# Kernel optimization log

Measured on AMD Instinct MI355X. Metric: run time of the kernel, lower is better.

## Reference

```python
import jax, jax.numpy as jnp
import numpy as np

N = 50000; F = 128; H = 128; E = 800000; G = 512; C = 1000; CE = 64; L = 128
EPS = 1e-5

def gcn_conv(x, src, dst, W, b, num_nodes):
    # PyG GCNConv: add self loops, sym-normalize, aggregate at dst
    loop = jnp.arange(num_nodes)
    s = jnp.concatenate([src, loop])
    d = jnp.concatenate([dst, loop])
    deg = jax.ops.segment_sum(jnp.ones_like(d, dtype=x.dtype), d, num_segments=num_nodes)
    dinv = jnp.where(deg > 0, jax.lax.rsqrt(deg), 0.0)
    norm = dinv[s] * dinv[d]                      # [E+N]
    h = x @ W                                     # [N,H]
    msg = h[s] * norm[:, None]                    # gather + scale
    return jax.ops.segment_sum(msg, d, num_segments=num_nodes) + b

def layer_norm(x, w, b):
    mu = jnp.mean(x, axis=-1, keepdims=True)
    var = jnp.var(x, axis=-1, keepdims=True)
    return (x - mu) * jax.lax.rsqrt(var + EPS) * w + b

def setup_inputs() -> dict:
    key = jax.random.key(0)
    ks = jax.random.split(key, 16)
    x = jax.random.normal(ks[0], (N, F), dtype=jnp.float32)
    edge_index = jax.random.randint(ks[1], (2, E), 0, N)
    batch = jnp.sort(jax.random.randint(ks[2], (N,), 0, G))
    cell_lines = jax.random.randint(ks[3], (G,), 0, C)
    def kai(k, shape):
        fan_in = shape[0]
        bound = np.sqrt(6.0 / fan_in)
        return jax.random.uniform(k, shape, jnp.float32, -bound, bound)
    return {
        'x': x, 'edge_index': edge_index, 'batch': batch, 'cell_lines': cell_lines,
        'W1': kai(ks[4], (F, H)), 'b1': jnp.zeros((H,), jnp.float32),
        'W2': kai(ks[5], (H, H)), 'b2': jnp.zeros((H,), jnp.float32),
        'emb': jax.random.normal(ks[6], (C, CE), dtype=jnp.float32),
        'Wc': kai(ks[7], (H + CE, H)), 'bc': jnp.zeros((H,), jnp.float32),
        'lnc_w': jnp.ones((H,), jnp.float32), 'lnc_b': jnp.zeros((H,), jnp.float32),
        'Wf1': kai(ks[8], (H, H)), 'bf1': jnp.zeros((H,), jnp.float32),
        'ln1_w': jnp.ones((H,), jnp.float32), 'ln1_b': jnp.zeros((H,), jnp.float32),
        'Wf2': kai(ks[9], (H, L)), 'bf2': jnp.zeros((L,), jnp.float32),
    }

def reference(x, edge_index, batch, cell_lines, W1, b1, W2, b2, emb, Wc, bc,
              lnc_w, lnc_b, Wf1, bf1, ln1_w, ln1_b, Wf2, bf2):
    src, dst = edge_index[0], edge_index[1]
    h = jax.nn.relu(gcn_conv(x, src, dst, W1, b1, N))
    h = jax.nn.relu(gcn_conv(h, src, dst, W2, b2, N))
    g = jax.ops.segment_sum(h, batch, num_segments=G)          # global_add_pool [G,H]
    ce = emb[cell_lines]                                       # [G,CE]
    comb = jnp.concatenate([g, ce], axis=1)
    comb = jax.nn.relu(layer_norm(comb @ Wc + bc, lnc_w, lnc_b))
    out = jax.nn.relu(comb @ Wf1 + bf1)                        # dropout = identity (eval)
    out = layer_norm(out, ln1_w, ln1_b)
    return out @ Wf2 + bf2
```

## Files before the change

### kernel.cpp

```cpp
#include <hip/hip_runtime.h>

#define N_NODES 50000
#define NFEAT 128
#define NEDGE 800000
#define NGRAPH 512
#define NCE 64
#define EPS 1e-5f
#define NBUCK 196
#define EPB 4096
#define BCAP 6144

typedef short s8v __attribute__((ext_vector_type(8)));
typedef float f4v __attribute__((ext_vector_type(4)));
typedef float f2v __attribute__((ext_vector_type(2)));

static __device__ __forceinline__ unsigned short f2bf(float f) {
    unsigned int u = __float_as_uint(f);
    unsigned int r = u + 0x7fffu + ((u >> 16) & 1u);
    return (unsigned short)(r >> 16);
}
static __device__ __forceinline__ float bf_lo(unsigned int packed) {
    return __uint_as_float(packed << 16);
}
static __device__ __forceinline__ float bf_hi(unsigned int packed) {
    return __uint_as_float(packed & 0xffff0000u);
}
static __device__ __forceinline__ float bf_us(unsigned short us) {
    return __uint_as_float(((unsigned int)us) << 16);
}
static __device__ __forceinline__ f2v unpk(unsigned int u) {
    f2v r; r.x = bf_lo(u); r.y = bf_hi(u); return r;
}

__global__ __launch_bounds__(256) void wcast_kernel(
    const float* __restrict__ W1, const float* __restrict__ W2,
    unsigned short* __restrict__ WT1, unsigned short* __restrict__ WT2,
    int* __restrict__ bucketCursor)
{
    if (blockIdx.x == 0 && blockIdx.y == 0 && threadIdx.x < NBUCK)
        bucketCursor[threadIdx.x] = 0;
    const float* W = blockIdx.y ? W2 : W1;
    unsigned short* WT = blockIdx.y ? WT2 : WT1;
    int idx = blockIdx.x * 256 + threadIdx.x;
    int k = idx >> 7, n = idx & 127;
    WT[n * 128 + k] = f2bf(W[idx]);
}

__global__ __launch_bounds__(256) void bucket_scatter_kernel(
    const int* __restrict__ ei, int* __restrict__ bucketCursor,
    unsigned int* __restrict__ recbuf, int E)
{
    __shared__ int hist[NBUCK];
    __shared__ int lbase[NBUCK];
    __shared__ int gbase[NBUCK];
    __shared__ int cur[NBUCK];
    __shared__ int scanbuf[256];
    __shared__ unsigned int staging[EPB];
    int tid = threadIdx.x;
    if (tid < NBUCK) { hist[tid] = 0; cur[tid] = 0; }
    __syncthreads();

    unsigned int rec[EPB / 256];
    int e0 = blockIdx.x * EPB + tid;
#pragma unroll
    for (int i = 0; i < EPB / 256; ++i) {
        int e = e0 + i * 256;
        if (e < E) {
            unsigned int sv = (unsigned)ei[e];
            unsigned int dv = (unsigned)ei[E + e];
            rec[i] = sv | (dv << 16);
            atomicAdd(&hist[dv >> 8], 1);
        } else {
            rec[i] = 0xffffffffu;
        }
    }
    __syncthreads();
    int v = (tid < NBUCK) ? hist[tid] : 0;
    scanbuf[tid] = v; __syncthreads();
    for (int off = 1; off < 256; off <<= 1) {
        int t = (tid >= off) ? scanbuf[tid - off] : 0;
        __syncthreads();
        scanbuf[tid] += t;
        __syncthreads();
    }
    if (tid < NBUCK) lbase[tid] = scanbuf[tid] - v;
    int total = scanbuf[255];
    if (tid < NBUCK) gbase[tid] = (v > 0) ? atomicAdd(&bucketCursor[tid], v) : 0;
    __syncthreads();
#pragma unroll
    for (int i = 0; i < EPB / 256; ++i) {
        if (rec[i] != 0xffffffffu) {
            int b = rec[i] >> 24;
            int loc = atomicAdd(&cur[b], 1);
            staging[lbase[b] + loc] = rec[i];
        }
    }
    __syncthreads();
    for (int s = tid; s < total; s += 256) {
        unsigned int r = staging[s];
        int b = r >> 24;
        int pos = gbase[b] + (s - lbase[b]);
        if (pos < BCAP) recbuf[(size_t)b * BCAP + pos] = r;
    }
}

__global__ __launch_bounds__(256) void bucket_csr_kernel(
    const unsigned int* __restrict__ recbuf, const int* __restrict__ bucketCursor,
    int* __restrict__ rowbeg, unsigned short* __restrict__ deg,
    float* __restrict__ dinv, unsigned short* __restrict__ colidx)
{
    __shared__ int cnt[256];
    __shared__ int cur[256];
    __shared__ int scanbuf[256];
    __shared__ unsigned short stage[BCAP];
    int b = blockIdx.x, tid = threadIdx.x;
    int base = b * BCAP;
    int len = bucketCursor[b]; if (len > BCAP) len = BCAP;
    cnt[tid] = 0;
    __syncthreads();
    for (int s = tid; s < len; s += 256) {
        unsigned int r = recbuf[base + s];
        atomicAdd(&cnt[(r >> 16) & 255], 1);
    }
    __syncthreads();
    int v = cnt[tid];
    scanbuf[tid] = v; __syncthreads();
    for (int off = 1; off < 256; off <<= 1) {
        int t = (tid >= off) ? scanbuf[tid - off] : 0;
        __syncthreads();
        scanbuf[tid] += t;
        __syncthreads();
    }
    int excl = scanbuf[tid] - v;
    int node = b * 256 + tid;
    if (node < N_NODES) {
        rowbeg[node] = base + excl;
        deg[node] = (unsigned short)v;
        dinv[node] = rsqrtf((float)v + 1.0f);
    }
    cur[tid] = excl;
    __syncthreads();
    for (int s = tid; s < len; s += 256) {
        unsigned int r = recbuf[base + s];
        int pos = atomicAdd(&cur[(r >> 16) & 255], 1);
        stage[pos] = (unsigned short)(r & 0xffffu);
    }
    __syncthreads();
    for (int s = tid; s < len; s += 256) colidx[base + s] = stage[s];
}

template<bool FP32IN>
__global__ __launch_bounds__(256) void gemm_mfma_kernel(
    const void* __restrict__ Ain, const unsigned short* __restrict__ WTg,
    const float* __restrict__ dinv, unsigned short* __restrict__ HS, int nrows)
{
    __shared__ unsigned short as[128 * 128];
    __shared__ unsigned short wt[128 * 128];
    const int tid = threadIdx.x;
    const int row0 = blockIdx.x * 128;

    {
        const uint4* src = reinterpret_cast<const uint4*>(WTg);
        uint4* dst = reinterpret_cast<uint4*>(wt);
#pragma unroll
        for (int i = 0; i < 8; ++i) dst[tid + i * 256] = src[tid + i * 256];
    }
    if (FP32IN) {
        const float* X = (const float*)Ain;
#pragma unroll
        for (int i = 0; i < 16; ++i) {
            int f = tid + i * 256;
            int r = f >> 5, c4 = f & 31;
            int rr = row0 + r; if (rr >= nrows) rr = nrows - 1;
            float4 v = *reinterpret_cast<const float4*>(&X[rr * 128 + c4 * 4]);
            ushort4 o;
            o.x = f2bf(v.x); o.y = f2bf(v.y); o.z = f2bf(v.z); o.w = f2bf(v.w);
            *reinterpret_cast<ushort4*>(&as[r * 128 + c4 * 4]) = o;
        }
    } else {
        const unsigned short* X = (const unsigned short*)Ain;
#pragma unroll
        for (int i = 0; i < 8; ++i) {
            int f = tid + i * 256;
            int r = f >> 4, c8 = f & 15;
            int rr = row0 + r; if (rr >= nrows) rr = nrows - 1;
            *reinterpret_cast<uint4*>(&as[r * 128 + c8 * 8]) =
                *reinterpret_cast<const uint4*>(&X[rr * 128 + c8 * 8]);
        }
    }
    __syncthreads();

    const int w = tid >> 6;
    const int lane = tid & 63;
    const int quad = lane >> 4;
    const int col0 = lane & 15;

    s8v afr[2][4];
#pragma unroll
    for (int rt = 0; rt < 2; ++rt)
#pragma unroll
        for (int kt = 0; kt < 4; ++kt)
            afr[rt][kt] = *reinterpret_cast<const s8v*>(
                &as[(w * 32 + rt * 16 + col0) * 128 + kt * 32 + quad * 8]);

    f4v acc[2][8];
#pragma unroll
    for (int rt = 0; rt < 2; ++rt)
#pragma unroll
        for (int nt = 0; nt < 8; ++nt)
            acc[rt][nt] = (f4v){0.f, 0.f, 0.f, 0.f};

#pragma unroll
    for (int nt = 0; nt < 8; ++nt) {
        s8v bfr[4];
#pragma unroll
        for (int kt = 0; kt < 4; ++kt)
            bfr[kt] = *reinterpret_cast<const s8v*>(
                &wt[(nt * 16 + col0) * 128 + kt * 32 + quad * 8]);
#pragma unroll
        for (int rt = 0; rt < 2; ++rt)
#pragma unroll
            for (int kt = 0; kt < 4; ++kt)
                acc[rt][nt] = __builtin_amdgcn_mfma_f32_16x16x32_bf16(
                    afr[rt][kt], bfr[kt], acc[rt][nt], 0, 0, 0);
    }

    float dv[2][4];
#pragma unroll
    for (int rt = 0; rt < 2; ++rt)
#pragma unroll
        for (int reg = 0; reg < 4; ++reg) {
            int r = row0 + w * 32 + rt * 16 + quad * 4 + reg;
            dv[rt][reg] = (r < nrows) ? dinv[r] : 0.f;
        }

#pragma unroll
    for (int rt = 0; rt < 2; ++rt)
#pragma unroll
        for (int nt = 0; nt < 8; ++nt)
#pragma unroll
            for (int reg = 0; reg < 4; ++reg) {
                int rl = w * 32 + rt * 16 + quad * 4 + reg;
                as[rl * 128 + nt * 16 + col0] = f2bf(acc[rt][nt][reg] * dv[rt][reg]);
            }
    __syncthreads();
#pragma unroll
    for (int i = 0; i < 8; ++i) {
        int f = tid + i * 256;
        int r = f >> 4, c8 = f & 15;
        if (row0 + r < nrows)
            *reinterpret_cast<uint4*>(&HS[(size_t)(row0 + r) * 128 + c8 * 8]) =
                *reinterpret_cast<const uint4*>(&as[r * 128 + c8 * 8]);
    }
}

static __device__ __forceinline__ uint2 agg_node(
    const uint2* __restrict__ H2, const int* __restrict__ rowbeg,
    const unsigned short* __restrict__ deg, const unsigned short* __restrict__ colidx,
    const float* __restrict__ dinv, const float* __restrict__ bias,
    int node, int lane)
{
    const int half = lane >> 5;
    const int sub = lane & 31;
    const int beg = rowbeg[node];
    const int cnt = (int)deg[node] + 1;
    f2v a01 = {0.f, 0.f}, a23 = {0.f, 0.f};
    f2v b01 = {0.f, 0.f}, b23 = {0.f, 0.f};
    for (int base = 0; base < cnt; base += 64) {
        int m = cnt - base; if (m > 64) m = 64;
        int p = base + lane;
        int idx = 0;
        if (lane < m) idx = (p == 0) ? node : (int)colidx[beg + p - 1];
        int j = 0;
        for (; j + 16 <= m; j += 16) {
            uint2 t[8];
#pragma unroll
            for (int q = 0; q < 8; ++q) {
                int u = __shfl(idx, j + q * 2 + half);
                t[q] = H2[(size_t)u * 32 + sub];
            }
#pragma unroll
            for (int q = 0; q < 8; q += 2) {
                a01 += unpk(t[q].x);     a23 += unpk(t[q].y);
                b01 += unpk(t[q + 1].x); b23 += unpk(t[q + 1].y);
            }
        }
        for (; j + 4 <= m; j += 4) {
            int ua = __shfl(idx, j + half);
            int ub = __shfl(idx, j + 2 + half);
            uint2 ta = H2[(size_t)ua * 32 + sub];
            uint2 tb = H2[(size_t)ub * 32 + sub];
            a01 += unpk(ta.x); a23 += unpk(ta.y);
            b01 += unpk(tb.x); b23 += unpk(tb.y);
        }
        if (j + 2 <= m) {
            int u = __shfl(idx, j + half);
            uint2 t = H2[(size_t)u * 32 + sub];
            a01 += unpk(t.x); a23 += unpk(t.y);
            j += 2;
        }
        if (j < m) {
            int u = __shfl(idx, j);
            uint2 t; t.x = 0u; t.y = 0u;
            if (half == 0) t = H2[(size_t)u * 32 + sub];
            a01 += unpk(t.x); a23 += unpk(t.y);
        }
    }
    a01 += b01; a23 += b23;
    float s0 = a01.x + __shfl_xor(a01.x, 32);
    float s1 = a01.y + __shfl_xor(a01.y, 32);
    float s2 = a23.x + __shfl_xor(a23.x, 32);
    float s3 = a23.y + __shfl_xor(a23.y, 32);
    float sc = dinv[node];
    float4 bv = *reinterpret_cast<const float4*>(&bias[sub * 4]);
    float o0 = fmaxf(fmaf(s0, sc, bv.x), 0.f);
    float o1 = fmaxf(fmaf(s1, sc, bv.y), 0.f);
    float o2 = fmaxf(fmaf(s2, sc, bv.z), 0.f);
    float o3 = fmaxf(fmaf(s3, sc, bv.w), 0.f);
    uint2 o;
    o.x = (unsigned int)f2bf(o0) | ((unsigned int)f2bf(o1) << 16);
    o.y = (unsigned int)f2bf(o2) | ((unsigned int)f2bf(o3) << 16);
    return o;
}

__global__ __launch_bounds__(256) void aggregate_kernel(
    const uint2* __restrict__ H2,
    const int* __restrict__ rowbeg, const unsigned short* __restrict__ deg,
    const unsigned short* __restrict__ colidx,
    const float* __restrict__ dinv, const float* __restrict__ bias,
    uint2* __restrict__ OUT, int n)
{
    int wid = (blockIdx.x * blockDim.x + threadIdx.x) >> 6;
    int lane = threadIdx.x & 63;
    if (wid >= n) return;
    uint2 o = agg_node(H2, rowbeg, deg, colidx, dinv, bias, wid, lane);
    if ((lane >> 5) == 0) OUT[(size_t)wid * 32 + (lane & 31)] = o;
}

__global__ __launch_bounds__(1024, 8) void fused_agg_gemm_kernel(
    const uint2* __restrict__ H2, const int* __restrict__ rowbeg,
    const unsigned short* __restrict__ deg, const unsigned short* __restrict__ colidx,
    const float* __restrict__ dinv, const float* __restrict__ bias,
    const unsigned short* __restrict__ WTg, unsigned short* __restrict__ HS2, int n)
{
    __shared__ unsigned short as[128 * 128];
    __shared__ unsigned short wt[128 * 128];
    const int tid = threadIdx.x;
    const int row0 = blockIdx.x * 128;

    {
        const uint4* src = reinterpret_cast<const uint4*>(WTg);
        uint4* dst = reinterpret_cast<uint4*>(wt);
        dst[tid] = src[tid];
        dst[tid + 1024] = src[tid + 1024];
    }

    const int w16 = tid >> 6;
    const int lane = tid & 63;

    uint2* asu2 = reinterpret_cast<uint2*>(as);
#pragma unroll 1
    for (int i = 0; i < 8; ++i) {
        int r = w16 * 8 + i;
        int node = row0 + r;
        if (node < n) {
            uint2 o = agg_node(H2, rowbeg, deg, colidx, dinv, bias, node, lane);
            if ((lane >> 5) == 0) asu2[r * 32 + (lane & 31)] = o;
        }
    }
    __syncthreads();

    const int quad = lane >> 4;
    const int col0 = lane & 15;
    const int wr  = w16 >> 1;
    const int nt0 = (w16 & 1) * 4;

    s8v afr[4];
#pragma unroll
    for (int kt = 0; kt < 4; ++kt)
        afr[kt] = *reinterpret_cast<const s8v*>(
            &as[(wr * 16 + col0) * 128 + kt * 32 + quad * 8]);

    f4v acc[4];
#pragma unroll
    for (int nt = 0; nt < 4; ++nt) acc[nt] = (f4v){0.f, 0.f, 0.f, 0.f};

#pragma unroll
    for (int nt = 0; nt < 4; ++nt) {
        s8v bfr[4];
#pragma unroll
        for (int kt = 0; kt < 4; ++kt)
            bfr[kt] = *reinterpret_cast<const s8v*>(
                &wt[((nt0 + nt) * 16 + col0) * 128 + kt * 32 + quad * 8]);
#pragma unroll
        for (int kt = 0; kt < 4; ++kt)
            acc[nt] = __builtin_amdgcn_mfma_f32_16x16x32_bf16(
                afr[kt], bfr[kt], acc[nt], 0, 0, 0);
    }

    float dv[4];
#pragma unroll
    for (int reg = 0; reg < 4; ++reg) {
        int r = row0 + wr * 16 + quad * 4 + reg;
        dv[reg] = (r < n) ? dinv[r] : 0.f;
    }
    __syncthreads();
#pragma unroll
    for (int nt = 0; nt < 4; ++nt)
#pragma unroll
        for (int reg = 0; reg < 4; ++reg)
            as[(wr * 16 + quad * 4 + reg) * 128 + (nt0 + nt) * 16 + col0] =
                f2bf(acc[nt][reg] * dv[reg]);
    __syncthreads();
#pragma unroll
    for (int i = 0; i < 2; ++i) {
        int f = tid + i * 1024;
        int r = f >> 4, c8 = f & 15;
        if (row0 + r < n)
            *reinterpret_cast<uint4*>(&HS2[(size_t)(row0 + r) * 128 + c8 * 8]) =
                *reinterpret_cast<const uint4*>(&as[r * 128 + c8 * 8]);
    }
}

__global__ __launch_bounds__(256) void tail_kernel(
    const unsigned short* __restrict__ h2b, const int* __restrict__ batch,
    const int* __restrict__ cell, const float* __restrict__ emb,
    const float* __restrict__ Wc, const float* __restrict__ bc,
    const float* __restrict__ lncw, const float* __restrict__ lncb,
    const float* __restrict__ Wf1, const float* __restrict__ bf1,
    const float* __restrict__ ln1w, const float* __restrict__ ln1b,
    const float* __restrict__ Wf2, const float* __restrict__ bf2,
    float* __restrict__ out)
{
    __shared__ __align__(16) float comb[192];
    __shared__ __align__(16) float part[8][132];
    __shared__ float red[4];
    __shared__ __align__(16) float vec[128];
    const int gi = blockIdx.x;
    const int tid = threadIdx.x;
    const int cg = tid & 31;
    const int ks = tid >> 5;

    int lo = 0, hi = N_NODES;
    while (lo < hi) { int mid = (lo + hi) >> 1; if (batch[mid] < gi) lo = mid + 1; else hi = mid; }
    int lo2 = lo, hi2 = N_NODES;
    while (lo2 < hi2) { int mid = (lo2 + hi2) >> 1; if (batch[mid] < gi + 1) lo2 = mid + 1; else hi2 = mid; }

    {
        int q = tid >> 6;
        int j = tid & 63;
        const unsigned int* h2u = (const unsigned int*)h2b;
        f2v acc = {0.f, 0.f};
        for (int v = lo + q; v < lo2; v += 4)
            acc += unpk(h2u[(size_t)v * 64 + j]);
        part[q][j * 2]     = acc.x;
        part[q][j * 2 + 1] = acc.y;
    }
    __syncthreads();
    if (tid < 128) comb[tid] = (part[0][tid] + part[1][tid]) + (part[2][tid] + part[3][tid]);
    else if (tid < 192) comb[tid] = emb[cell[gi] * 64 + (tid - 128)];
    __syncthreads();

    {
        float c[24];
#pragma unroll
        for (int i = 0; i < 6; ++i) {
            float4 t = *reinterpret_cast<const float4*>(&comb[ks * 24 + i * 4]);
            c[i * 4 + 0] = t.x; c[i * 4 + 1] = t.y; c[i * 4 + 2] = t.z; c[i * 4 + 3] = t.w;
        }
        float a0 = 0.f, a1 = 0.f, a2 = 0.f, a3 = 0.f;
#pragma unroll
        for (int i = 0; i < 24; ++i) {
            const float4 w = *reinterpret_cast<const float4*>(&Wc[(ks * 24 + i) * 128 + cg * 4]);
            a0 = fmaf(c[i], w.x, a0);
            a1 = fmaf(c[i], w.y, a1);
            a2 = fmaf(c[i], w.z, a2);
            a3 = fmaf(c[i], w.w, a3);
        }
        float4 o; o.x = a0; o.y = a1; o.z = a2; o.w = a3;
        *reinterpret_cast<float4*>(&part[ks][cg * 4]) = o;
    }
    __syncthreads();
    {
        float y = 0.f;
        if (tid < 128) {
            y = bc[tid];
#pragma unroll
            for (int s = 0; s < 8; ++s) y += part[s][tid];
        }
        float s1 = (tid < 128) ? y : 0.f;
        float s2 = (tid < 128) ? y * y : 0.f;
        if (tid < 128) {
#pragma unroll
            for (int off = 32; off > 0; off >>= 1) {
                s1 += __shfl_down(s1, off);
                s2 += __shfl_down(s2, off);
            }
            if ((tid & 63) == 0) { red[(tid >> 6) * 2] = s1; red[(tid >> 6) * 2 + 1] = s2; }
        }
        __syncthreads();
        float mu = (red[0] + red[2]) * (1.f / 128.f);
        float ms = (red[1] + red[3]) * (1.f / 128.f);
        float var = ms - mu * mu;
        if (tid < 128) {
            float yv = (y - mu) * rsqrtf(var + EPS) * lncw[tid] + lncb[tid];
            vec[tid] = fmaxf(yv, 0.f);
        }
    }
    __syncthreads();

    {
        float c[16];
#pragma unroll
        for (int i = 0; i < 4; ++i) {
            float4 t = *reinterpret_cast<const float4*>(&vec[ks * 16 + i * 4]);
            c[i * 4 + 0] = t.x; c[i * 4 + 1] = t.y; c[i * 4 + 2] = t.z; c[i * 4 + 3] = t.w;
        }
        float a0 = 0.f, a1 = 0.f, a2 = 0.f, a3 = 0.f;
#pragma unroll
        for (int i = 0; i < 16; ++i) {
            const float4 w = *reinterpret_cast<const float4*>(&Wf1[(ks * 16 + i) * 128 + cg * 4]);
            a0 = fmaf(c[i], w.x, a0);
            a1 = fmaf(c[i], w.y, a1);
            a2 = fmaf(c[i], w.z, a2);
            a3 = fmaf(c[i], w.w, a3);
        }
        float4 o; o.x = a0; o.y = a1; o.z = a2; o.w = a3;
        *reinterpret_cast<float4*>(&part[ks][cg * 4]) = o;
    }
    __syncthreads();
    {
        float y = 0.f;
        if (tid < 128) {
            y = bf1[tid];
#pragma unroll
            for (int s = 0; s < 8; ++s) y += part[s][tid];
            y = fmaxf(y, 0.f);
        }
        float s1 = (tid < 128) ? y : 0.f;
        float s2 = (tid < 128) ? y * y : 0.f;
        if (tid < 128) {
#pragma unroll
            for (int off = 32; off > 0; off >>= 1) {
                s1 += __shfl_down(s1, off);
                s2 += __shfl_down(s2, off);
            }
            if ((tid & 63) == 0) { red[(tid >> 6) * 2] = s1; red[(tid >> 6) * 2 + 1] = s2; }
        }
        __syncthreads();
        float mu = (red[0] + red[2]) * (1.f / 128.f);
        float ms = (red[1] + red[3]) * (1.f / 128.f);
        float var = ms - mu * mu;
        if (tid < 128)
            vec[tid] = (y - mu) * rsqrtf(var + EPS) * ln1w[tid] + ln1b[tid];
    }
    __syncthreads();

    {
        float c[16];
#pragma unroll
        for (int i = 0; i < 4; ++i) {
            float4 t = *reinterpret_cast<const float4*>(&vec[ks * 16 + i * 4]);
            c[i * 4 + 0] = t.x; c[i * 4 + 1] = t.y; c[i * 4 + 2] = t.z; c[i * 4 + 3] = t.w;
        }
        float a0 = 0.f, a1 = 0.f, a2 = 0.f, a3 = 0.f;
#pragma unroll
        for (int i = 0; i < 16; ++i) {
            const float4 w = *reinterpret_cast<const float4*>(&Wf2[(ks * 16 + i) * 128 + cg * 4]);
            a0 = fmaf(c[i], w.x, a0);
            a1 = fmaf(c[i], w.y, a1);
            a2 = fmaf(c[i], w.z, a2);
            a3 = fmaf(c[i], w.w, a3);
        }
        float4 o; o.x = a0; o.y = a1; o.z = a2; o.w = a3;
        *reinterpret_cast<float4*>(&part[ks][cg * 4]) = o;
    }
    __syncthreads();
    if (tid < 128) {
        float y = bf2[tid];
#pragma unroll
        for (int s = 0; s < 8; ++s) y += part[s][tid];
        out[gi * 128 + tid] = y;
    }
}

extern "C" void kernel_launch(void* const* d_in, const int* in_sizes, int n_in,
                              void* d_out, int out_size, void* d_ws, size_t ws_size,
                              hipStream_t stream) {
    const float* x    = (const float*)d_in[0];
    const int*   ei   = (const int*)d_in[1];
    const int*   batch= (const int*)d_in[2];
    const int*   cell = (const int*)d_in[3];
    const float* W1   = (const float*)d_in[4];
    const float* b1   = (const float*)d_in[5];
    const float* W2   = (const float*)d_in[6];
    const float* b2   = (const float*)d_in[7];
    const float* emb  = (const float*)d_in[8];
    const float* Wc   = (const float*)d_in[9];
    const float* bc   = (const float*)d_in[10];
    const float* lncw = (const float*)d_in[11];
    const float* lncb = (const float*)d_in[12];
    const float* Wf1  = (const float*)d_in[13];
    const float* bf1  = (const float*)d_in[14];
    const float* ln1w = (const float*)d_in[15];
    const float* ln1b = (const float*)d_in[16];
    const float* Wf2  = (const float*)d_in[17];
    const float* bf2  = (const float*)d_in[18];
    float* out = (float*)d_out;

    char* ws = (char*)d_ws;
    size_t off = 0;
    auto alloc = [&](size_t bytes) { char* p = ws + off; off = (off + bytes + 255) & ~size_t(255); return p; };
    float*          dinv        = (float*)alloc(N_NODES * 4);
    int*            rowbeg      = (int*)  alloc(N_NODES * 4);
    unsigned short* deg         = (unsigned short*)alloc(N_NODES * 2);
    unsigned short* colidx      = (unsigned short*)alloc((size_t)NBUCK * BCAP * 2);
    int*            bucketCursor= (int*)  alloc(NBUCK * 4);
    unsigned int*   recbuf      = (unsigned int*)alloc((size_t)NBUCK * BCAP * 4);
    unsigned short* wt1         = (unsigned short*)alloc(128 * 128 * 2);
    unsigned short* wt2         = (unsigned short*)alloc(128 * 128 * 2);
    unsigned short* hs          = (unsigned short*)alloc((size_t)N_NODES * 128 * 2);
    unsigned short* hs2         = (unsigned short*)alloc((size_t)N_NODES * 128 * 2);
    unsigned short* h2b         = (unsigned short*)alloc((size_t)N_NODES * 128 * 2);

    const int nbEdge = (NEDGE + EPB - 1) / EPB;
    const int nbGemm = (N_NODES + 127) / 128;
    const int nbAgg  = (N_NODES + 3) / 4;

    wcast_kernel<<<dim3(64, 2), 256, 0, stream>>>(W1, W2, wt1, wt2, bucketCursor);

    bucket_scatter_kernel<<<nbEdge, 256, 0, stream>>>(ei, bucketCursor, recbuf, NEDGE);
    bucket_csr_kernel<<<NBUCK, 256, 0, stream>>>(recbuf, bucketCursor, rowbeg, deg, dinv, colidx);

    gemm_mfma_kernel<true><<<nbGemm, 256, 0, stream>>>(x, wt1, dinv, hs, N_NODES);

    fused_agg_gemm_kernel<<<nbGemm, 1024, 0, stream>>>(
        (const uint2*)hs, rowbeg, deg, colidx, dinv, b1, wt2, hs2, N_NODES);

    aggregate_kernel<<<nbAgg, 256, 0, stream>>>((const uint2*)hs2, rowbeg, deg, colidx,
                                                dinv, b2, (uint2*)h2b, N_NODES);
    tail_kernel<<<NGRAPH, 256, 0, stream>>>(h2b, batch, cell, emb, Wc, bc, lncw, lncb,
                                            Wf1, bf1, ln1w, ln1b, Wf2, bf2, out);
}
```

Baseline: 231.3 us.

## Fuse second-layer aggregation with global add pool and merge weight-cast launch

Replaces the standalone second aggregation kernel with a 128-node-tile kernel. It aggregates into shared memory, reduces each tile per graph id, and atomically adds the sums into a pooled fp32 buffer. The tail kernel then reads pooled sums directly, so the bf16 node-feature buffer is no longer written and re-read and the per-graph binary search is gone. The weight cast is folded into extra blocks of the edge-scatter kernel, and a memset zeroes the cursors and pooled buffer. Rows in the fused agg+GEMM kernel are now handed out through a shared atomic counter to balance uneven degrees. In exchange it adds float atomics with nondeterministic summation order and per-tile graph loops with barriers.

```diff
diff --git a/kernel.cpp b/kernel.cpp
--- a/kernel.cpp
+++ b/kernel.cpp
@@ -32,23 +32,11 @@
     f2v r; r.x = bf_lo(u); r.y = bf_hi(u); return r;
 }
 
-__global__ __launch_bounds__(256) void wcast_kernel(
+__global__ __launch_bounds__(256) void scatter_wcast_kernel(
+    const int* __restrict__ ei, int* __restrict__ bucketCursor,
+    unsigned int* __restrict__ recbuf, int E,
     const float* __restrict__ W1, const float* __restrict__ W2,
-    unsigned short* __restrict__ WT1, unsigned short* __restrict__ WT2,
-    int* __restrict__ bucketCursor)
-{
-    if (blockIdx.x == 0 && blockIdx.y == 0 && threadIdx.x < NBUCK)
-        bucketCursor[threadIdx.x] = 0;
-    const float* W = blockIdx.y ? W2 : W1;
-    unsigned short* WT = blockIdx.y ? WT2 : WT1;
-    int idx = blockIdx.x * 256 + threadIdx.x;
-    int k = idx >> 7, n = idx & 127;
-    WT[n * 128 + k] = f2bf(W[idx]);
-}
-
-__global__ __launch_bounds__(256) void bucket_scatter_kernel(
-    const int* __restrict__ ei, int* __restrict__ bucketCursor,
-    unsigned int* __restrict__ recbuf, int E)
+    unsigned short* __restrict__ WT1, unsigned short* __restrict__ WT2)
 {
     __shared__ int hist[NBUCK];
     __shared__ int lbase[NBUCK];
@@ -57,6 +45,17 @@
     __shared__ int scanbuf[256];
     __shared__ unsigned int staging[EPB];
     int tid = threadIdx.x;
+
+    if (blockIdx.x >= NBUCK) {
+        int b = blockIdx.x - NBUCK;
+        const float* W = (b >= 64) ? W2 : W1;
+        unsigned short* WT = (b >= 64) ? WT2 : WT1;
+        int idx = (b & 63) * 256 + tid;
+        int k = idx >> 7, n2 = idx & 127;
+        WT[n2 * 128 + k] = f2bf(W[idx]);
+        return;
+    }
+
     if (tid < NBUCK) { hist[tid] = 0; cur[tid] = 0; }
     __syncthreads();
 
@@ -323,20 +322,6 @@
     return o;
 }
 
-__global__ __launch_bounds__(256) void aggregate_kernel(
-    const uint2* __restrict__ H2,
-    const int* __restrict__ rowbeg, const unsigned short* __restrict__ deg,
-    const unsigned short* __restrict__ colidx,
-    const float* __restrict__ dinv, const float* __restrict__ bias,
-    uint2* __restrict__ OUT, int n)
-{
-    int wid = (blockIdx.x * blockDim.x + threadIdx.x) >> 6;
-    int lane = threadIdx.x & 63;
-    if (wid >= n) return;
-    uint2 o = agg_node(H2, rowbeg, deg, colidx, dinv, bias, wid, lane);
-    if ((lane >> 5) == 0) OUT[(size_t)wid * 32 + (lane & 31)] = o;
-}
-
 __global__ __launch_bounds__(1024, 8) void fused_agg_gemm_kernel(
     const uint2* __restrict__ H2, const int* __restrict__ rowbeg,
     const unsigned short* __restrict__ deg, const unsigned short* __restrict__ colidx,
@@ -345,27 +330,32 @@
 {
     __shared__ unsigned short as[128 * 128];
     __shared__ unsigned short wt[128 * 128];
+    __shared__ int nodeCur;
     const int tid = threadIdx.x;
     const int row0 = blockIdx.x * 128;
 
+    if (tid == 0) nodeCur = 0;
     {
         const uint4* src = reinterpret_cast<const uint4*>(WTg);
         uint4* dst = reinterpret_cast<uint4*>(wt);
         dst[tid] = src[tid];
         dst[tid + 1024] = src[tid + 1024];
     }
+    __syncthreads();
 
     const int w16 = tid >> 6;
     const int lane = tid & 63;
 
     uint2* asu2 = reinterpret_cast<uint2*>(as);
-#pragma unroll 1
-    for (int i = 0; i < 8; ++i) {
-        int r = w16 * 8 + i;
-        int node = row0 + r;
+    for (;;) {
+        int rr = 0;
+        if (lane == 0) rr = atomicAdd(&nodeCur, 1);
+        rr = __shfl(rr, 0);
+        if (rr >= 128) break;
+        int node = row0 + rr;
         if (node < n) {
             uint2 o = agg_node(H2, rowbeg, deg, colidx, dinv, bias, node, lane);
-            if ((lane >> 5) == 0) asu2[r * 32 + (lane & 31)] = o;
+            if ((lane >> 5) == 0) asu2[rr * 32 + (lane & 31)] = o;
         }
     }
     __syncthreads();
@@ -422,8 +412,60 @@
     }
 }
 
+__global__ __launch_bounds__(1024, 8) void agg_pool_kernel(
+    const uint2* __restrict__ H2, const int* __restrict__ rowbeg,
+    const unsigned short* __restrict__ deg, const unsigned short* __restrict__ colidx,
+    const float* __restrict__ dinv, const float* __restrict__ bias,
+    const int* __restrict__ batch, float* __restrict__ pooled, int n)
+{
+    __shared__ unsigned short as[128 * 128];
+    __shared__ int bsh[128];
+    __shared__ float psum[8][132];
+    __shared__ int nodeCur;
+    const int tid = threadIdx.x;
+    const int row0 = blockIdx.x * 128;
+    if (tid == 0) nodeCur = 0;
+    if (tid < 128) bsh[tid] = (row0 + tid < n) ? batch[row0 + tid] : -1;
+    __syncthreads();
+
+    const int lane = tid & 63;
+    uint2* asu2 = reinterpret_cast<uint2*>(as);
+    for (;;) {
+        int rr = 0;
+        if (lane == 0) rr = atomicAdd(&nodeCur, 1);
+        rr = __shfl(rr, 0);
+        if (rr >= 128) break;
+        int node = row0 + rr;
+        if (node < n) {
+            uint2 o = agg_node(H2, rowbeg, deg, colidx, dinv, bias, node, lane);
+            if ((lane >> 5) == 0) asu2[rr * 32 + (lane & 31)] = o;
+        }
+    }
+    __syncthreads();
+
+    const int g0 = bsh[0];
+    int last = row0 + 127; if (last > n - 1) last = n - 1;
+    const int g1 = batch[last];
+    const int s = tid >> 7;
+    const int f = tid & 127;
+    for (int g = g0; g <= g1; ++g) {
+        float acc = 0.f;
+        for (int r = s; r < 128; r += 8)
+            if (bsh[r] == g) acc += bf_us(as[r * 128 + f]);
+        psum[s][f] = acc;
+        __syncthreads();
+        if (tid < 128) {
+            float tot = 0.f;
+#pragma unroll
+            for (int q = 0; q < 8; ++q) tot += psum[q][f];
+            atomicAdd(&pooled[g * 128 + f], tot);
+        }
+        __syncthreads();
+    }
+}
+
 __global__ __launch_bounds__(256) void tail_kernel(
-    const unsigned short* __restrict__ h2b, const int* __restrict__ batch,
+    const float* __restrict__ pooled,
     const int* __restrict__ cell, const float* __restrict__ emb,
     const float* __restrict__ Wc, const float* __restrict__ bc,
     const float* __restrict__ lncw, const float* __restrict__ lncb,
@@ -441,23 +483,7 @@
     const int cg = tid & 31;
     const int ks = tid >> 5;
 
-    int lo = 0, hi = N_NODES;
-    while (lo < hi) { int mid = (lo + hi) >> 1; if (batch[mid] < gi) lo = mid + 1; else hi = mid; }
-    int lo2 = lo, hi2 = N_NODES;
-    while (lo2 < hi2) { int mid = (lo2 + hi2) >> 1; if (batch[mid] < gi + 1) lo2 = mid + 1; else hi2 = mid; }
-
-    {
-        int q = tid >> 6;
-        int j = tid & 63;
-        const unsigned int* h2u = (const unsigned int*)h2b;
-        f2v acc = {0.f, 0.f};
-        for (int v = lo + q; v < lo2; v += 4)
-            acc += unpk(h2u[(size_t)v * 64 + j]);
-        part[q][j * 2]     = acc.x;
-        part[q][j * 2 + 1] = acc.y;
-    }
-    __syncthreads();
-    if (tid < 128) comb[tid] = (part[0][tid] + part[1][tid]) + (part[2][tid] + part[3][tid]);
+    if (tid < 128) comb[tid] = pooled[gi * 128 + tid];
     else if (tid < 192) comb[tid] = emb[cell[gi] * 64 + (tid - 128)];
     __syncthreads();
 
@@ -611,25 +637,25 @@
     char* ws = (char*)d_ws;
     size_t off = 0;
     auto alloc = [&](size_t bytes) { char* p = ws + off; off = (off + bytes + 255) & ~size_t(255); return p; };
+    int*            bucketCursor= (int*)  alloc(1024);
+    float*          pooled      = (float*)alloc((size_t)NGRAPH * 128 * 4);
     float*          dinv        = (float*)alloc(N_NODES * 4);
     int*            rowbeg      = (int*)  alloc(N_NODES * 4);
     unsigned short* deg         = (unsigned short*)alloc(N_NODES * 2);
     unsigned short* colidx      = (unsigned short*)alloc((size_t)NBUCK * BCAP * 2);
-    int*            bucketCursor= (int*)  alloc(NBUCK * 4);
     unsigned int*   recbuf      = (unsigned int*)alloc((size_t)NBUCK * BCAP * 4);
     unsigned short* wt1         = (unsigned short*)alloc(128 * 128 * 2);
     unsigned short* wt2         = (unsigned short*)alloc(128 * 128 * 2);
     unsigned short* hs          = (unsigned short*)alloc((size_t)N_NODES * 128 * 2);
     unsigned short* hs2         = (unsigned short*)alloc((size_t)N_NODES * 128 * 2);
-    unsigned short* h2b         = (unsigned short*)alloc((size_t)N_NODES * 128 * 2);
 
     const int nbEdge = (NEDGE + EPB - 1) / EPB;
     const int nbGemm = (N_NODES + 127) / 128;
-    const int nbAgg  = (N_NODES + 3) / 4;
-
-    wcast_kernel<<<dim3(64, 2), 256, 0, stream>>>(W1, W2, wt1, wt2, bucketCursor);
-
-    bucket_scatter_kernel<<<nbEdge, 256, 0, stream>>>(ei, bucketCursor, recbuf, NEDGE);
+
+    hipMemsetAsync(bucketCursor, 0, 1024 + (size_t)NGRAPH * 128 * 4, stream);
+
+    scatter_wcast_kernel<<<nbEdge + 128, 256, 0, stream>>>(ei, bucketCursor, recbuf, NEDGE,
+                                                           W1, W2, wt1, wt2);
     bucket_csr_kernel<<<NBUCK, 256, 0, stream>>>(recbuf, bucketCursor, rowbeg, deg, dinv, colidx);
 
     gemm_mfma_kernel<true><<<nbGemm, 256, 0, stream>>>(x, wt1, dinv, hs, N_NODES);
@@ -637,8 +663,9 @@
     fused_agg_gemm_kernel<<<nbGemm, 1024, 0, stream>>>(
         (const uint2*)hs, rowbeg, deg, colidx, dinv, b1, wt2, hs2, N_NODES);
 
-    aggregate_kernel<<<nbAgg, 256, 0, stream>>>((const uint2*)hs2, rowbeg, deg, colidx,
-                                                dinv, b2, (uint2*)h2b, N_NODES);
-    tail_kernel<<<NGRAPH, 256, 0, stream>>>(h2b, batch, cell, emb, Wc, bc, lncw, lncb,
+    agg_pool_kernel<<<nbGemm, 1024, 0, stream>>>(
+        (const uint2*)hs2, rowbeg, deg, colidx, dinv, b2, batch, pooled, N_NODES);
+
+    tail_kernel<<<NGRAPH, 256, 0, stream>>>(pooled, cell, emb, Wc, bc, lncw, lncb,
                                             Wf1, bf1, ln1w, ln1b, Wf2, bf2, out);
 }
```

After: 221.6 us. 4.2% less time.
